# Kernel optimization log

Measured on AMD Instinct MI355X. Metric: run time of the kernel, lower is better.

## Reference

```python
import jax, jax.numpy as jnp
import numpy as np
import math

B, S, D, H = 4, 2048, 1024, 16
DK = D // H

def setup_inputs() -> dict:
    key = jax.random.key(0)
    ks = jax.random.split(key, 6)
    scale = 1.0 / math.sqrt(D)
    x = jax.random.normal(ks[0], (B, S, D), dtype=jnp.float32)
    mask = jnp.tril(jnp.ones((S, S), dtype=jnp.int32))[None, None]  # [1,1,S,S] causal
    Wq = jax.random.normal(ks[1], (D, D), dtype=jnp.float32) * scale
    Wk = jax.random.normal(ks[2], (D, D), dtype=jnp.float32) * scale
    Wv = jax.random.normal(ks[3], (D, D), dtype=jnp.float32) * scale
    Wo = jax.random.normal(ks[4], (D, D), dtype=jnp.float32) * scale
    z = jnp.zeros((D,), dtype=jnp.float32)
    return {"x": x, "mask": mask, "Wq": Wq, "bq": z, "Wk": Wk, "bk": z,
            "Wv": Wv, "bv": z, "Wo": Wo, "bo": z}

def reference(x, mask, Wq, bq, Wk, bk, Wv, bv, Wo, bo):
    bsz, seq_len, d_model = x.shape
    def split_heads(t):  # [B,S,D] -> [B,H,S,DK]
        return t.reshape(bsz, seq_len, H, DK).transpose(0, 2, 1, 3)
    Q = split_heads(x @ Wq + bq)
    K = split_heads(x @ Wk + bk)
    V = split_heads(x @ Wv + bv)
    scores = jnp.einsum('bhqd,bhkd->bhqk', Q, K) / jnp.sqrt(jnp.asarray(DK, x.dtype))
    scores = jnp.where(mask == 0, jnp.asarray(-jnp.inf, x.dtype), scores)
    attn = jax.nn.softmax(scores, axis=-1)
    # dropout is identity in eval mode
    context = jnp.einsum('bhqk,bhkd->bhqd', attn, V)
    context = context.transpose(0, 2, 1, 3).reshape(bsz, seq_len, d_model)
    return context @ Wo + bo
```

## Files before the change

kernel.cpp:

```cpp
#include <hip/hip_runtime.h>
#include <hip/hip_bf16.h>
#include <math.h>

#define BATCH 4
#define SEQ   2048
#define DMODEL 1024
#define NHEAD 16
#define DHEAD 64
#define MROWS (BATCH * SEQ)
#define SC_Q  0.1803368801111244f

typedef __attribute__((ext_vector_type(8))) short short8;
typedef __attribute__((ext_vector_type(4))) float f32x4;
typedef __attribute__((ext_vector_type(4))) unsigned short ushort4v;

__device__ inline unsigned short f2bf(float f) {
    union { float f; unsigned int u; } v; v.f = f;
    unsigned int r = v.u + 0x7FFFu + ((v.u >> 16) & 1u);
    return (unsigned short)(r >> 16);
}

__device__ inline unsigned int cvt_pk_bf16(float a, float b) {
    unsigned int r;
    asm("v_cvt_pk_bf16_f32 %0, %1, %2" : "=v"(r) : "v"(a), "v"(b));
    return r;
}

__device__ __forceinline__ void g2l16(const unsigned short* g, unsigned short* l) {
    __builtin_amdgcn_global_load_lds(
        (const __attribute__((address_space(1))) unsigned int*)g,
        (__attribute__((address_space(3))) unsigned int*)l, 16, 0, 0);
}

#define SBAR()  do { __builtin_amdgcn_s_barrier(); asm volatile("" ::: "memory"); } while (0)

__global__ __launch_bounds__(256) void cvt_bf16_kernel(
    const float* __restrict__ src, unsigned short* __restrict__ dst, int n4)
{
    const int i = blockIdx.x * 256 + threadIdx.x;
    if (i < n4) {
        float4 v = ((const float4*)src)[i];
        ushort4v o = { f2bf(v.x), f2bf(v.y), f2bf(v.z), f2bf(v.w) };
        ((ushort4v*)dst)[i] = o;
    }
}

__global__ __launch_bounds__(256) void bias_pack_kernel(
    const float* __restrict__ bq, const float* __restrict__ bk,
    const float* __restrict__ bv, float* __restrict__ b3)
{
    const int i = blockIdx.x * 256 + threadIdx.x;
    if (i < DMODEL) {
        b3[i]              = bq[i];
        b3[i + DMODEL]     = bk[i];
        b3[i + 2 * DMODEL] = bv[i];
    }
}

__global__ __launch_bounds__(256) void transpose_cvt_kernel(
    const float* __restrict__ W0, const float* __restrict__ W1,
    const float* __restrict__ W2, const float* __restrict__ W3,
    unsigned short* __restrict__ T0, unsigned short* __restrict__ T1,
    unsigned short* __restrict__ T2, unsigned short* __restrict__ T3)
{
    const float* W; unsigned short* T;
    switch (blockIdx.z) {
        case 0: W = W0; T = T0; break;
        case 1: W = W1; T = T1; break;
        case 2: W = W2; T = T2; break;
        default: W = W3; T = T3; break;
    }
    __shared__ float tile[32][33];
    const int r0 = blockIdx.y * 32, c0 = blockIdx.x * 32;
    const int c = threadIdx.x & 31, r = threadIdx.x >> 5;
    #pragma unroll
    for (int i = 0; i < 4; ++i)
        tile[r + i * 8][c] = W[(size_t)(r0 + r + i * 8) * DMODEL + c0 + c];
    __syncthreads();
    #pragma unroll
    for (int i = 0; i < 4; ++i)
        T[(size_t)(c0 + r + i * 8) * DMODEL + r0 + c] = f2bf(tile[c][r + i * 8]);
}

__global__ __launch_bounds__(256) void transpose_v_kernel(
    const unsigned short* __restrict__ Vin, unsigned short* __restrict__ Vt)
{
    __shared__ unsigned short t[64][72];
    const int tid = threadIdx.x;
    const int kt = blockIdx.x, bh = blockIdx.y;
    const unsigned short* src = Vin + ((size_t)bh * SEQ + kt * 64) * DHEAD;
    const int r = tid >> 3, c = (tid & 7) * 8;
    *(short8*)&t[r][c]      = *(const short8*)(src + (size_t)r * DHEAD + c);
    *(short8*)&t[r + 32][c] = *(const short8*)(src + (size_t)(r + 32) * DHEAD + c);
    __syncthreads();
    unsigned short* dst = Vt + (size_t)bh * DHEAD * SEQ + kt * 64;
    const int d = tid >> 3, p0 = (tid & 7) * 8;
    short8 v0, v1;
    #pragma unroll
    for (int i = 0; i < 8; ++i) {
        const int p = p0 + i;
        const int k = (p & 32) | (((p >> 2) & 1) << 4) | (((p >> 3) & 3) << 2) | (p & 3);
        v0[i] = (short)t[k][d];
        v1[i] = (short)t[k][d + 32];
    }
    *(short8*)(dst + (size_t)d * SEQ + p0)        = v0;
    *(short8*)(dst + (size_t)(d + 32) * SEQ + p0) = v1;
}

__device__ __forceinline__ void gemm_main_8ph(
    const unsigned short* __restrict__ A, const unsigned short* __restrict__ Bt,
    f32x4 (&acc)[4][4], int m0, int n0, int wm, int wn, int l15, int quad)
{
    __shared__ unsigned short As[3][256 * 64];
    __shared__ unsigned short Bs[3][128 * 64];

    const int tid = threadIdx.x;

    #pragma unroll
    for (int i = 0; i < 4; ++i)
        #pragma unroll
        for (int j = 0; j < 4; ++j) acc[i][j] = (f32x4){0.f, 0.f, 0.f, 0.f};

    const unsigned short* gA[4];
    const unsigned short* gB[2];
    int cA[4], cB[2];
    #pragma unroll
    for (int j = 0; j < 4; ++j) {
        const int c = tid + j * 512, row = c >> 3, gq = (c & 7) ^ (row & 7);
        gA[j] = A + (size_t)(m0 + row) * DMODEL + gq * 8;
        cA[j] = c * 8;
    }
    #pragma unroll
    for (int j = 0; j < 2; ++j) {
        const int c = tid + j * 512, row = c >> 3, gq = (c & 7) ^ (row & 7);
        gB[j] = Bt + (size_t)(n0 + row) * DMODEL + gq * 8;
        cB[j] = c * 8;
    }

    #pragma unroll
    for (int tt = 0; tt < 2; ++tt) {
        #pragma unroll
        for (int j = 0; j < 4; ++j) { g2l16(gA[j], &As[tt][cA[j]]); gA[j] += 64; }
        #pragma unroll
        for (int j = 0; j < 2; ++j) { g2l16(gB[j], &Bs[tt][cB[j]]); gB[j] += 64; }
    }
    asm volatile("s_waitcnt vmcnt(6)" ::: "memory");
    SBAR();

    const int rm[4] = { wm + l15, wm + 16 + l15, wm + 32 + l15, wm + 48 + l15 };
    const int rn[4] = { wn + l15, wn + 16 + l15, wn + 32 + l15, wn + 48 + l15 };

    int cur = 0, sb = 2;
    #pragma unroll 1
    for (int t = 0; t < DMODEL / 64; ++t) {
        const unsigned short* As_c = &As[cur][0];
        const unsigned short* Bs_c = &Bs[cur][0];
        unsigned short* As_s = &As[sb][0];
        unsigned short* Bs_s = &Bs[sb][0];
        const bool st = (t < DMODEL / 64 - 2);

        short8 af[4], bfr[4];

        #pragma unroll
        for (int i = 0; i < 4; ++i) {
            af[i]  = *(const short8*)&As_c[rm[i] * 64 + (quad ^ (rm[i] & 7)) * 8];
            bfr[i] = *(const short8*)&Bs_c[rn[i] * 64 + (quad ^ (rn[i] & 7)) * 8];
        }
        if (st) { g2l16(gA[0], &As_s[cA[0]]); gA[0] += 64;
                  g2l16(gA[1], &As_s[cA[1]]); gA[1] += 64;
                  g2l16(gA[2], &As_s[cA[2]]); gA[2] += 64; }
        SBAR();
        __builtin_amdgcn_s_setprio(1);
        #pragma unroll
        for (int mi = 0; mi < 4; ++mi)
            #pragma unroll
            for (int ni = 0; ni < 4; ++ni)
                acc[mi][ni] = __builtin_amdgcn_mfma_f32_16x16x32_bf16(
                    af[mi], bfr[ni], acc[mi][ni], 0, 0, 0);
        __builtin_amdgcn_s_setprio(0);
        SBAR();

        #pragma unroll
        for (int i = 0; i < 4; ++i) {
            af[i]  = *(const short8*)&As_c[rm[i] * 64 + ((4 + quad) ^ (rm[i] & 7)) * 8];
            bfr[i] = *(const short8*)&Bs_c[rn[i] * 64 + ((4 + quad) ^ (rn[i] & 7)) * 8];
        }
        if (st) { g2l16(gA[3], &As_s[cA[3]]); gA[3] += 64;
                  g2l16(gB[0], &Bs_s[cB[0]]); gB[0] += 64;
                  g2l16(gB[1], &Bs_s[cB[1]]); gB[1] += 64; }
        if (st)
            asm volatile("s_waitcnt vmcnt(6)" ::: "memory");
        else if (t == DMODEL / 64 - 2)
            asm volatile("s_waitcnt vmcnt(0)" ::: "memory");
        SBAR();
        __builtin_amdgcn_s_setprio(1);
        #pragma unroll
        for (int mi = 0; mi < 4; ++mi)
            #pragma unroll
            for (int ni = 0; ni < 4; ++ni)
                acc[mi][ni] = __builtin_amdgcn_mfma_f32_16x16x32_bf16(
                    af[mi], bfr[ni], acc[mi][ni], 0, 0, 0);
        __builtin_amdgcn_s_setprio(0);
        SBAR();

        cur = (cur == 2) ? 0 : cur + 1;
        sb  = (sb  == 2) ? 0 : sb  + 1;
    }
}

__global__ __launch_bounds__(512, 2) void gemm_qkv(
    const unsigned short* __restrict__ A, const unsigned short* __restrict__ Bt,
    const float* __restrict__ bias3, unsigned short* __restrict__ QKV )
{
    const int tid  = threadIdx.x;
    const int wave = tid >> 6, lane = tid & 63;
    const int l15  = lane & 15, quad = lane >> 4;
    const int wm   = (wave >> 1) * 64;
    const int wn   = (wave & 1) * 64;
    const int m0   = blockIdx.y * 256;
    const int n0   = blockIdx.x * 128;

    f32x4 acc[4][4];
    gemm_main_8ph(A, Bt, acc, m0, n0, wm, wn, l15, quad);

    const size_t elems = (size_t)MROWS * DMODEL;
    #pragma unroll
    for (int mi = 0; mi < 4; ++mi) {
        #pragma unroll
        for (int r = 0; r < 4; ++r) {
            const int m = m0 + wm + mi * 16 + quad * 4 + r;
            const int b = m >> 11, s = m & 2047;
            #pragma unroll
            for (int ni = 0; ni < 4; ++ni) {
                const int n   = n0 + wn + ni * 16 + l15;
                const int seg = n >> 10, nn = n & 1023;
                const int h = nn >> 6, dk = nn & 63;
                const float sc  = (seg == 0) ? SC_Q : 1.0f;
                const float val = (acc[mi][ni][r] + bias3[n]) * sc;
                QKV[seg * elems + (((size_t)(b * NHEAD + h)) * SEQ + s) * DHEAD + dk] = f2bf(val);
            }
        }
    }
}

__global__ __launch_bounds__(512, 2) void gemm_out(
    const unsigned short* __restrict__ A, const unsigned short* __restrict__ Bt,
    const float* __restrict__ bias, float* __restrict__ Cout)
{
    const int tid  = threadIdx.x;
    const int wave = tid >> 6, lane = tid & 63;
    const int l15  = lane & 15, quad = lane >> 4;
    const int wm   = (wave >> 1) * 64;
    const int wn   = (wave & 1) * 64;
    const int m0   = blockIdx.y * 256;
    const int n0   = blockIdx.x * 128;

    f32x4 acc[4][4];
    gemm_main_8ph(A, Bt, acc, m0, n0, wm, wn, l15, quad);

    #pragma unroll
    for (int mi = 0; mi < 4; ++mi) {
        #pragma unroll
        for (int r = 0; r < 4; ++r) {
            const int m = m0 + wm + mi * 16 + quad * 4 + r;
            #pragma unroll
            for (int ni = 0; ni < 4; ++ni) {
                const int n = n0 + wn + ni * 16 + l15;
                Cout[(size_t)m * DMODEL + n] = acc[mi][ni][r] + bias[n];
            }
        }
    }
}

__global__ __launch_bounds__(256, 4) void attn_mfma7(
    const unsigned short* __restrict__ Q, const unsigned short* __restrict__ K,
    const unsigned short* __restrict__ VtG, unsigned short* __restrict__ ctx_out)
{
    __shared__ alignas(16) unsigned short Ks[2][64 * 64];
    __shared__ alignas(16) unsigned short Vs[2][64 * 64];

    const int tid  = threadIdx.x;
    const int wave = tid >> 6, lane = tid & 63;
    const int l15  = lane & 15, quad = lane >> 4;
    const int qa   = blockIdx.x;
    const int qb   = 31 - qa;
    const int bh   = blockIdx.y;
    const int b    = bh >> 4, h = bh & 15;

    const unsigned short* Kb0 = K   + (size_t)bh * SEQ * DHEAD;
    const unsigned short* Vb0 = VtG + (size_t)bh * DHEAD * SEQ;

    short8 qf[2][2];
    #pragma unroll
    for (int g = 0; g < 2; ++g) {
        const int qtile = g ? qb : qa;
        const unsigned short* qrow =
            Q + ((size_t)bh * SEQ + qtile * 64 + wave * 16 + l15) * DHEAD + quad * 8;
        qf[g][0] = *(const short8*)qrow;
        qf[g][1] = *(const short8*)(qrow + 32);
    }

    f32x4 Of[2][4];
    float lsum[2] = {0.f, 0.f};
    #pragma unroll
    for (int g = 0; g < 2; ++g)
        #pragma unroll
        for (int i = 0; i < 4; ++i) Of[g][i] = (f32x4){0.f, 0.f, 0.f, 0.f};

    const int qloc = wave * 16 + l15;
    const f32x4 zero4 = (f32x4){0.f, 0.f, 0.f, 0.f};

    const int ck0 = tid >> 3, cg0 = tid & 7;
    const int ck1 = (tid + 256) >> 3, cg1 = tid & 7;

    #define STAGE(buf, jb)                                                          \
        do {                                                                        \
            const unsigned short* Kt_ = Kb0 + (size_t)(jb) * 64 * DHEAD;            \
            const unsigned short* Vt_ = Vb0 + (jb) * 64;                            \
            g2l16(Kt_ + (size_t)ck0 * DHEAD + (cg0 ^ (ck0 & 7)) * 8,                \
                  &Ks[buf][(tid) * 8]);                                             \
            g2l16(Vt_ + (size_t)ck0 * SEQ   + (cg0 ^ (ck0 & 7)) * 8,                \
                  &Vs[buf][(tid) * 8]);                                             \
            g2l16(Kt_ + (size_t)ck1 * DHEAD + (cg1 ^ (ck1 & 7)) * 8,                \
                  &Ks[buf][(tid + 256) * 8]);                                       \
            g2l16(Vt_ + (size_t)ck1 * SEQ   + (cg1 ^ (ck1 & 7)) * 8,                \
                  &Vs[buf][(tid + 256) * 8]);                                       \
        } while (0)

    STAGE(0, 0);

    for (int jb = 0; jb <= qb; ++jb) {
        const int cur = jb & 1;
        asm volatile("s_waitcnt vmcnt(0)" ::: "memory");
        __syncthreads();
        if (jb < qb) STAGE(cur ^ 1, jb + 1);

        const bool act0  = (jb <= qa);
        const bool diag0 = (jb == qa);
        const bool diag1 = (jb == qb);
        const unsigned short* KsC = &Ks[cur][0];
        const unsigned short* VsC = &Vs[cur][0];

        union { unsigned int u[4]; short8 v; } pa[2][2];
        #pragma unroll
        for (int nt = 0; nt < 4; ++nt) {
            const int k = nt * 16 + l15;
            const short8 a0 = *(const short8*)&KsC[(k * 8 + ( quad      ^ (k & 7))) * 8];
            const short8 a1 = *(const short8*)&KsC[(k * 8 + ((quad + 4) ^ (k & 7))) * 8];

            f32x4 s1 = __builtin_amdgcn_mfma_f32_16x16x32_bf16(a0, qf[1][0], zero4, 0, 0, 0);
            s1       = __builtin_amdgcn_mfma_f32_16x16x32_bf16(a1, qf[1][1], s1,    0, 0, 0);
            f32x4 p1;
            #pragma unroll
            for (int r = 0; r < 4; ++r) p1[r] = __builtin_amdgcn_exp2f(s1[r]);
            if (diag1) {
                #pragma unroll
                for (int r = 0; r < 4; ++r)
                    if (nt * 16 + quad * 4 + r > qloc) p1[r] = 0.f;
            }
            lsum[1] += (p1[0] + p1[1]) + (p1[2] + p1[3]);
            pa[1][nt >> 1].u[(nt & 1) * 2]     = cvt_pk_bf16(p1[0], p1[1]);
            pa[1][nt >> 1].u[(nt & 1) * 2 + 1] = cvt_pk_bf16(p1[2], p1[3]);

            if (act0) {
                f32x4 s0 = __builtin_amdgcn_mfma_f32_16x16x32_bf16(a0, qf[0][0], zero4, 0, 0, 0);
                s0       = __builtin_amdgcn_mfma_f32_16x16x32_bf16(a1, qf[0][1], s0,    0, 0, 0);
                f32x4 p0;
                #pragma unroll
                for (int r = 0; r < 4; ++r) p0[r] = __builtin_amdgcn_exp2f(s0[r]);
                if (diag0) {
                    #pragma unroll
                    for (int r = 0; r < 4; ++r)
                        if (nt * 16 + quad * 4 + r > qloc) p0[r] = 0.f;
                }
                lsum[0] += (p0[0] + p0[1]) + (p0[2] + p0[3]);
                pa[0][nt >> 1].u[(nt & 1) * 2]     = cvt_pk_bf16(p0[0], p0[1]);
                pa[0][nt >> 1].u[(nt & 1) * 2 + 1] = cvt_pk_bf16(p0[2], p0[3]);
            }
        }

        #pragma unroll
        for (int cc = 0; cc < 2; ++cc) {
            #pragma unroll
            for (int nt = 0; nt < 4; ++nt) {
                const int d = nt * 16 + l15;
                const short8 vb = *(const short8*)
                    &VsC[(d * 8 + ((cc * 4 + quad) ^ (d & 7))) * 8];
                Of[1][nt] = __builtin_amdgcn_mfma_f32_16x16x32_bf16(
                    pa[1][cc].v, vb, Of[1][nt], 0, 0, 0);
                if (act0)
                    Of[0][nt] = __builtin_amdgcn_mfma_f32_16x16x32_bf16(
                        pa[0][cc].v, vb, Of[0][nt], 0, 0, 0);
            }
        }
    }
    #undef STAGE

    #pragma unroll
    for (int g = 0; g < 2; ++g) {
        const int qtile = g ? qb : qa;
        float l = lsum[g];
        l += __shfl_xor(l, 16);
        l += __shfl_xor(l, 32);
        #pragma unroll
        for (int r = 0; r < 4; ++r) {
            const float inv = 1.0f / __shfl(l, quad * 4 + r);
            const int s = qtile * 64 + wave * 16 + quad * 4 + r;
            unsigned short* o = ctx_out + ((size_t)(b * SEQ + s)) * DMODEL + h * DHEAD;
            #pragma unroll
            for (int nt = 0; nt < 4; ++nt)
                o[nt * 16 + l15] = f2bf(Of[g][nt][r] * inv);
        }
    }
}

extern "C" void kernel_launch(void* const* d_in, const int* in_sizes, int n_in,
                              void* d_out, int out_size, void* d_ws, size_t ws_size,
                              hipStream_t stream) {
    const float* x  = (const float*)d_in[0];
    const float* Wq = (const float*)d_in[2];
    const float* bq = (const float*)d_in[3];
    const float* Wk = (const float*)d_in[4];
    const float* bk = (const float*)d_in[5];
    const float* Wv = (const float*)d_in[6];
    const float* bv = (const float*)d_in[7];
    const float* Wo = (const float*)d_in[8];
    const float* bo = (const float*)d_in[9];
    float* out = (float*)d_out;

    const size_t elems  = (size_t)MROWS * DMODEL;
    const size_t welems = (size_t)DMODEL * DMODEL;
    unsigned short* xbf   = (unsigned short*)d_ws;
    unsigned short* WqkvT = xbf + elems;
    unsigned short* WoT   = WqkvT + 3 * welems;
    unsigned short* Qbuf  = WoT + welems;
    unsigned short* Kbuf  = Qbuf + elems;
    unsigned short* Vbuf  = Kbuf + elems;
    unsigned short* VtG   = Vbuf + elems;
    unsigned short* Cbuf  = VtG + elems;
    float*          bias3 = (float*)(Cbuf + elems);

    dim3 blk(256);
    dim3 blk2(512);

    cvt_bf16_kernel<<<dim3((int)(elems / 4 / 256)), blk, 0, stream>>>(x, xbf, (int)(elems / 4));
    transpose_cvt_kernel<<<dim3(32, 32, 4), blk, 0, stream>>>(
        Wq, Wk, Wv, Wo, WqkvT, WqkvT + welems, WqkvT + 2 * welems, WoT);
    bias_pack_kernel<<<dim3(4), blk, 0, stream>>>(bq, bk, bv, bias3);

    dim3 gqkv(3 * DMODEL / 128, MROWS / 256);
    gemm_qkv<<<gqkv, blk2, 0, stream>>>(xbf, WqkvT, bias3, Qbuf);

    transpose_v_kernel<<<dim3(SEQ / 64, BATCH * NHEAD), blk, 0, stream>>>(Vbuf, VtG);

    dim3 gattn(16, BATCH * NHEAD);
    attn_mfma7<<<gattn, blk, 0, stream>>>(Qbuf, Kbuf, VtG, Cbuf);

    dim3 gout(DMODEL / 128, MROWS / 256);
    gemm_out<<<gout, blk2, 0, stream>>>(Cbuf, WoT, bo, out);
}
```

Before: 275.9 us.

## Use 256x256 double-buffered tile with staged loads for QKV projection GEMM

Replaces the shared 256x128 triple-buffered mainloop for the QKV GEMM with a dedicated 256x256 tile kernel. Each wave now computes 128x64 of output, and global-to-LDS loads are split into four phases interleaved with MFMA sub-blocks. The larger tile raises arithmetic intensity and halves the block count. In exchange it doubles accumulator registers per thread, which may limit occupancy at 2 blocks/CU, and it uses 128KB of LDS per block.

```diff
diff --git a/kernel.cpp b/kernel.cpp
--- a/kernel.cpp
+++ b/kernel.cpp
@@ -107,6 +107,162 @@
     *(short8*)(dst + (size_t)(d + 32) * SEQ + p0) = v1;
 }
 
+__global__ __launch_bounds__(512, 2) void gemm_qkv(
+    const unsigned short* __restrict__ A, const unsigned short* __restrict__ Bt,
+    const float* __restrict__ bias3, unsigned short* __restrict__ QKV )
+{
+    __shared__ unsigned short As[2][256 * 64];
+    __shared__ unsigned short Bs[2][256 * 64];
+
+    const int tid  = threadIdx.x;
+    const int wave = tid >> 6, lane = tid & 63;
+    const int l15  = lane & 15, quad = lane >> 4;
+    const int wm   = (wave >> 2) * 128;
+    const int wn   = (wave & 3) * 64;
+    const int m0   = blockIdx.y * 256;
+    const int n0   = blockIdx.x * 256;
+
+    f32x4 acc[8][4];
+    #pragma unroll
+    for (int i = 0; i < 8; ++i)
+        #pragma unroll
+        for (int j = 0; j < 4; ++j) acc[i][j] = (f32x4){0.f, 0.f, 0.f, 0.f};
+
+    const unsigned short* gA[2][2];
+    const unsigned short* gB[2][2];
+    int cO[2][2];
+    #pragma unroll
+    for (int h = 0; h < 2; ++h)
+        #pragma unroll
+        for (int j = 0; j < 2; ++j) {
+            const int c = j * 1024 + h * 512 + tid;
+            const int row = c >> 3, gq = (c & 7) ^ (row & 7);
+            cO[h][j] = c * 8;
+            gA[h][j] = A  + (size_t)(m0 + row) * DMODEL + gq * 8;
+            gB[h][j] = Bt + (size_t)(n0 + row) * DMODEL + gq * 8;
+        }
+
+    #define STG_A(buf, h) do {                                                 \
+        g2l16(gA[h][0], &As[buf][cO[h][0]]); gA[h][0] += 64;                   \
+        g2l16(gA[h][1], &As[buf][cO[h][1]]); gA[h][1] += 64; } while (0)
+    #define STG_B(buf, h) do {                                                 \
+        g2l16(gB[h][0], &Bs[buf][cO[h][0]]); gB[h][0] += 64;                   \
+        g2l16(gB[h][1], &Bs[buf][cO[h][1]]); gB[h][1] += 64; } while (0)
+
+    STG_B(0, 0); STG_B(0, 1); STG_A(0, 0); STG_A(0, 1);
+    asm volatile("s_waitcnt vmcnt(2)" ::: "memory");
+    SBAR();
+
+    const int NT = DMODEL / 64;
+    #pragma unroll 1
+    for (int t = 0; t < NT; ++t) {
+        const int cur = t & 1, nxt = cur ^ 1;
+        const unsigned short* As_c = &As[cur][0];
+        const unsigned short* Bs_c = &Bs[cur][0];
+        const bool st = (t + 1 < NT);
+
+        short8 bfr[4][2], af[4];
+
+        #pragma unroll
+        for (int ni = 0; ni < 4; ++ni) {
+            const int rn = wn + ni * 16 + l15;
+            bfr[ni][0] = *(const short8*)&Bs_c[rn * 64 + ((    quad) ^ (rn & 7)) * 8];
+            bfr[ni][1] = *(const short8*)&Bs_c[rn * 64 + ((4 + quad) ^ (rn & 7)) * 8];
+        }
+        #pragma unroll
+        for (int i = 0; i < 4; ++i) {
+            const int rm = wm + i * 16 + l15;
+            af[i] = *(const short8*)&As_c[rm * 64 + ((quad) ^ (rm & 7)) * 8];
+        }
+        if (st) STG_B(nxt, 0);
+        SBAR();
+        __builtin_amdgcn_s_setprio(1);
+        #pragma unroll
+        for (int i = 0; i < 4; ++i)
+            #pragma unroll
+            for (int ni = 0; ni < 4; ++ni)
+                acc[i][ni] = __builtin_amdgcn_mfma_f32_16x16x32_bf16(
+                    af[i], bfr[ni][0], acc[i][ni], 0, 0, 0);
+        __builtin_amdgcn_s_setprio(0);
+        SBAR();
+
+        #pragma unroll
+        for (int i = 0; i < 4; ++i) {
+            const int rm = wm + i * 16 + l15;
+            af[i] = *(const short8*)&As_c[rm * 64 + ((4 + quad) ^ (rm & 7)) * 8];
+        }
+        if (st) STG_B(nxt, 1);
+        SBAR();
+        __builtin_amdgcn_s_setprio(1);
+        #pragma unroll
+        for (int i = 0; i < 4; ++i)
+            #pragma unroll
+            for (int ni = 0; ni < 4; ++ni)
+                acc[i][ni] = __builtin_amdgcn_mfma_f32_16x16x32_bf16(
+                    af[i], bfr[ni][1], acc[i][ni], 0, 0, 0);
+        __builtin_amdgcn_s_setprio(0);
+        if (st) asm volatile("s_waitcnt vmcnt(4)" ::: "memory");
+        else    asm volatile("s_waitcnt vmcnt(0)" ::: "memory");
+        SBAR();
+
+        #pragma unroll
+        for (int i = 0; i < 4; ++i) {
+            const int rm = wm + 64 + i * 16 + l15;
+            af[i] = *(const short8*)&As_c[rm * 64 + ((quad) ^ (rm & 7)) * 8];
+        }
+        if (st) STG_A(nxt, 0);
+        SBAR();
+        __builtin_amdgcn_s_setprio(1);
+        #pragma unroll
+        for (int i = 0; i < 4; ++i)
+            #pragma unroll
+            for (int ni = 0; ni < 4; ++ni)
+                acc[4 + i][ni] = __builtin_amdgcn_mfma_f32_16x16x32_bf16(
+                    af[i], bfr[ni][0], acc[4 + i][ni], 0, 0, 0);
+        __builtin_amdgcn_s_setprio(0);
+        SBAR();
+
+        #pragma unroll
+        for (int i = 0; i < 4; ++i) {
+            const int rm = wm + 64 + i * 16 + l15;
+            af[i] = *(const short8*)&As_c[rm * 64 + ((4 + quad) ^ (rm & 7)) * 8];
+        }
+        if (st) STG_A(nxt, 1);
+        SBAR();
+        __builtin_amdgcn_s_setprio(1);
+        #pragma unroll
+        for (int i = 0; i < 4; ++i)
+            #pragma unroll
+            for (int ni = 0; ni < 4; ++ni)
+                acc[4 + i][ni] = __builtin_amdgcn_mfma_f32_16x16x32_bf16(
+                    af[i], bfr[ni][1], acc[4 + i][ni], 0, 0, 0);
+        __builtin_amdgcn_s_setprio(0);
+        if (st) asm volatile("s_waitcnt vmcnt(2)" ::: "memory");
+        SBAR();
+    }
+    #undef STG_A
+    #undef STG_B
+
+    const size_t elems = (size_t)MROWS * DMODEL;
+    #pragma unroll
+    for (int mi = 0; mi < 8; ++mi) {
+        #pragma unroll
+        for (int r = 0; r < 4; ++r) {
+            const int m = m0 + wm + mi * 16 + quad * 4 + r;
+            const int b = m >> 11, s = m & 2047;
+            #pragma unroll
+            for (int ni = 0; ni < 4; ++ni) {
+                const int n   = n0 + wn + ni * 16 + l15;
+                const int seg = n >> 10, nn = n & 1023;
+                const int h = nn >> 6, dk = nn & 63;
+                const float sc  = (seg == 0) ? SC_Q : 1.0f;
+                const float val = (acc[mi][ni][r] + bias3[n]) * sc;
+                QKV[seg * elems + (((size_t)(b * NHEAD + h)) * SEQ + s) * DHEAD + dk] = f2bf(val);
+            }
+        }
+    }
+}
+
 __device__ __forceinline__ void gemm_main_8ph(
     const unsigned short* __restrict__ A, const unsigned short* __restrict__ Bt,
     f32x4 (&acc)[4][4], int m0, int n0, int wm, int wn, int l15, int quad)
@@ -205,41 +361,6 @@
 
         cur = (cur == 2) ? 0 : cur + 1;
         sb  = (sb  == 2) ? 0 : sb  + 1;
-    }
-}
-
-__global__ __launch_bounds__(512, 2) void gemm_qkv(
-    const unsigned short* __restrict__ A, const unsigned short* __restrict__ Bt,
-    const float* __restrict__ bias3, unsigned short* __restrict__ QKV )
-{
-    const int tid  = threadIdx.x;
-    const int wave = tid >> 6, lane = tid & 63;
-    const int l15  = lane & 15, quad = lane >> 4;
-    const int wm   = (wave >> 1) * 64;
-    const int wn   = (wave & 1) * 64;
-    const int m0   = blockIdx.y * 256;
-    const int n0   = blockIdx.x * 128;
-
-    f32x4 acc[4][4];
-    gemm_main_8ph(A, Bt, acc, m0, n0, wm, wn, l15, quad);
-
-    const size_t elems = (size_t)MROWS * DMODEL;
-    #pragma unroll
-    for (int mi = 0; mi < 4; ++mi) {
-        #pragma unroll
-        for (int r = 0; r < 4; ++r) {
-            const int m = m0 + wm + mi * 16 + quad * 4 + r;
-            const int b = m >> 11, s = m & 2047;
-            #pragma unroll
-            for (int ni = 0; ni < 4; ++ni) {
-                const int n   = n0 + wn + ni * 16 + l15;
-                const int seg = n >> 10, nn = n & 1023;
-                const int h = nn >> 6, dk = nn & 63;
-                const float sc  = (seg == 0) ? SC_Q : 1.0f;
-                const float val = (acc[mi][ni][r] + bias3[n]) * sc;
-                QKV[seg * elems + (((size_t)(b * NHEAD + h)) * SEQ + s) * DHEAD + dk] = f2bf(val);
-            }
-        }
     }
 }
 
@@ -448,7 +569,7 @@
         Wq, Wk, Wv, Wo, WqkvT, WqkvT + welems, WqkvT + 2 * welems, WoT);
     bias_pack_kernel<<<dim3(4), blk, 0, stream>>>(bq, bk, bv, bias3);
 
-    dim3 gqkv(3 * DMODEL / 128, MROWS / 256);
+    dim3 gqkv(3 * DMODEL / 256, MROWS / 256);
     gemm_qkv<<<gqkv, blk2, 0, stream>>>(xbf, WqkvT, bias3, Qbuf);
 
     transpose_v_kernel<<<dim3(SEQ / 64, BATCH * NHEAD), blk, 0, stream>>>(Vbuf, VtG);
```

Measured after the change: 284.1 us. +3.0%, slower.
